# Kernel optimization log

Hardware: AMD Instinct MI355X
Metric: run time of the kernel (lower is better)

## Reference

```python
import jax, jax.numpy as jnp
import numpy as np

N_NODES = 150000
M_HYPEREDGES = 50000
N_TOTAL = N_NODES + M_HYPEREDGES
LATENT_DIM = 64
NUM_CLASS = 50
NNZ = 3_200_000
NUM_LAYERS = 3


def setup_inputs() -> dict:
    key = jax.random.key(0)
    k1, k2, k3, k4, k5, k6 = jax.random.split(key, 6)
    node_emb = 0.1 * jax.random.normal(k1, (N_NODES, LATENT_DIM), dtype=jnp.float32)
    hyper_emb = 0.1 * jax.random.normal(k2, (M_HYPEREDGES, LATENT_DIM), dtype=jnp.float32)
    W = jax.random.normal(k3, (LATENT_DIM, NUM_CLASS), dtype=jnp.float32) / np.sqrt(LATENT_DIM)
    b = jnp.zeros((NUM_CLASS,), dtype=jnp.float32)
    rows = jax.random.randint(k4, (NNZ,), 0, N_TOTAL, dtype=jnp.int32)
    cols = jax.random.randint(k5, (NNZ,), 0, N_TOTAL, dtype=jnp.int32)
    # normalized-adjacency-like small positive values
    vals = jax.random.uniform(k6, (NNZ,), dtype=jnp.float32) * 0.1
    return {"node_emb": node_emb, "hyper_emb": hyper_emb, "W": W, "b": b,
            "vals": vals, "rows": rows, "cols": cols}


def _spmm(vals, rows, cols, x):
    # y[r] = sum over edges (r, c): vals * x[c]   -- COO SpMM
    return jax.ops.segment_sum(vals[:, None] * x[cols], rows, num_segments=N_TOTAL)


def reference(node_emb, hyper_emb, W, b, vals, rows, cols):
    all_emb = jnp.concatenate([node_emb, hyper_emb], axis=0)  # [N, D]
    acc = all_emb  # running sum across layer embeddings (fused mean-pool)
    for _ in range(NUM_LAYERS):
        all_emb = _spmm(vals, rows, cols, all_emb)
        acc = acc + all_emb
    out = acc / (NUM_LAYERS + 1)          # mean over stacked layer embeddings
    nodes = out[:N_NODES]                 # split(out, [n_nodes, m_hyperedges])[0]
    Z = nodes @ W + b                     # linear head; dropout is identity in eval
    return jax.nn.log_softmax(Z, axis=1)
```

## Files before the change

kernel.cpp:

```cpp
#include <hip/hip_runtime.h>
#include <hip/hip_bf16.h>

#define N_NODES 150000
#define M_HYPER 50000
#define N_TOTAL 200000
#define DIM 64
#define NCLASS 50
#define NNZ 3200000

#define BSHIFT 9
#define BROWS 512
#define NBUK ((N_TOTAL + BROWS - 1) / BROWS)
#define EB 8192
#define CAP 9216

#define SCALE_UP 64.0f
#define SCALE_DN 0.015625f
#define VQ_ENC 163840.0f
#define VQ_DEC 6.103515625e-6f

typedef float v2f __attribute__((ext_vector_type(2)));

__global__ __launch_bounds__(512) void init_cur(int* __restrict__ bcur) {
    int t = threadIdx.x;
    if (t < NBUK) bcur[t] = t * CAP;
}

__global__ __launch_bounds__(1024) void bin_edges(
    const int* __restrict__ rows, const int* __restrict__ cols,
    const float* __restrict__ vals, int* __restrict__ bcur,
    int2* __restrict__ recs) {
    __shared__ int h[NBUK];
    __shared__ int lbase[NBUK];
    int base = blockIdx.x * EB;
    int cntE = NNZ - base; if (cntE > EB) cntE = EB;
    for (int i = threadIdx.x; i < NBUK; i += 1024) h[i] = 0;
    __syncthreads();
    for (int i = threadIdx.x; i < cntE; i += 1024)
        atomicAdd(&h[rows[base + i] >> BSHIFT], 1);
    __syncthreads();
    for (int i = threadIdx.x; i < NBUK; i += 1024) {
        int c = h[i];
        lbase[i] = c ? atomicAdd(&bcur[i], c) : 0;
    }
    __syncthreads();
    for (int i = threadIdx.x; i < NBUK; i += 1024) h[i] = 0;
    __syncthreads();
    for (int i = threadIdx.x; i < cntE; i += 1024) {
        int e = base + i;
        int r = rows[e];
        int b = r >> BSHIFT;
        int p = lbase[b] + atomicAdd(&h[b], 1);
        int q = __float2int_rn(vals[e] * VQ_ENC);
        if (q > 16383) q = 16383;
        if (p < NBUK * CAP)
            recs[p] = make_int2(((r & (BROWS - 1)) << 18) | cols[e], q);
    }
}

__global__ __launch_bounds__(512) void cnt_scan(const int* __restrict__ bcur,
                                                int* __restrict__ boff) {
    __shared__ int sh[512];
    int t = threadIdx.x;
    int c = (t < NBUK) ? (bcur[t] - t * CAP) : 0;
    sh[t] = c;
    __syncthreads();
    for (int off = 1; off < 512; off <<= 1) {
        int v = (t >= off) ? sh[t - off] : 0;
        __syncthreads();
        sh[t] += v;
        __syncthreads();
    }
    if (t < NBUK) boff[t] = sh[t] - c;
    if (t == 0) boff[NBUK] = NNZ;
}

__global__ __launch_bounds__(512) void build_csr(const int* __restrict__ boff,
                                                 const int2* __restrict__ recs,
                                                 int* __restrict__ row_ptr,
                                                 unsigned* __restrict__ edges) {
    __shared__ int h[BROWS * 8];
    __shared__ int ps[512];
    int b = blockIdx.x, t = threadIdx.x;
    int rbase = b * CAP;
    int obase = boff[b];
    int cnt = boff[b + 1] - obase;
    int row0 = b << BSHIFT;
    int nrows = N_TOTAL - row0;
    if (nrows > BROWS) nrows = BROWS;
    for (int i = t; i < BROWS * 8; i += 512) h[i] = 0;
    __syncthreads();
    for (int i = t; i < cnt; i += 512) {
        int rx = recs[rbase + i].x;
        int key = ((rx >> 18) << 3) | ((rx & 0x3FFFF) >> 15);
        atomicAdd(&h[key], 1);
    }
    __syncthreads();
    int loc[8];
    int s = 0;
#pragma unroll
    for (int j = 0; j < 8; ++j) { loc[j] = h[8 * t + j]; s += loc[j]; }
    ps[t] = s;
    __syncthreads();
    for (int off = 1; off < 512; off <<= 1) {
        int a = (t >= off) ? ps[t - off] : 0;
        __syncthreads();
        ps[t] += a;
        __syncthreads();
    }
    int run = obase + ((t == 0) ? 0 : ps[t - 1]);
    if (t < nrows) row_ptr[row0 + t] = run;
    if (b == NBUK - 1 && t == 0) row_ptr[N_TOTAL] = NNZ;
#pragma unroll
    for (int j = 0; j < 8; ++j) { h[8 * t + j] = run; run += loc[j]; }
    __syncthreads();
    for (int i = t; i < cnt; i += 512) {
        int2 rc = recs[rbase + i];
        int key = ((rc.x >> 18) << 3) | ((rc.x & 0x3FFFF) >> 15);
        int p = atomicAdd(&h[key], 1);
        edges[p] = (unsigned)(rc.x & 0x3FFFF) | ((unsigned)rc.y << 18);
    }
}

__global__ __launch_bounds__(256) void build_x_fp8(
    const float* __restrict__ node_emb, const float* __restrict__ hyper_emb,
    unsigned* __restrict__ xb) {
    int i = blockIdx.x * 256 + threadIdx.x;
    size_t base = (size_t)i * 4;
    const size_t NN = (size_t)N_NODES * DIM;
    if (base >= (size_t)N_TOTAL * DIM) return;
    float4 f;
    if (base < NN)
        f = *reinterpret_cast<const float4*>(node_emb + base);
    else
        f = *reinterpret_cast<const float4*>(hyper_emb + (base - NN));
    int lo = __builtin_amdgcn_cvt_pk_fp8_f32(f.x * SCALE_UP, f.y * SCALE_UP,
                                             0, false);
    int w = __builtin_amdgcn_cvt_pk_fp8_f32(f.z * SCALE_UP, f.w * SCALE_UP,
                                            lo, true);
    xb[i] = (unsigned)w;
}

__global__ __launch_bounds__(256) void spmm_gather(
    const int* __restrict__ row_ptr, const unsigned* __restrict__ edges,
    const unsigned char* __restrict__ x, unsigned char* __restrict__ y,
    int nrows) {
    int gid = blockIdx.x * 256 + threadIdx.x;
    int row = gid >> 4;
    int lane = threadIdx.x & 15;
    if (row >= nrows) return;
    int beg = row_ptr[row], end = row_ptr[row + 1];
    float a0 = 0.f, a1 = 0.f, a2 = 0.f, a3 = 0.f;
    int k = beg;
    for (; k + 7 < end; k += 8) {
        unsigned e[8];
        unsigned g[8];
#pragma unroll
        for (int j = 0; j < 8; ++j) e[j] = edges[k + j];
#pragma unroll
        for (int j = 0; j < 8; ++j)
            g[j] = *(const unsigned*)(x + ((size_t)(e[j] & 0x3FFFFu) << 6) + lane * 4);
#pragma unroll
        for (int j = 0; j < 8; ++j) {
            float v = (float)(e[j] >> 18) * VQ_DEC;
            v2f lo = __builtin_amdgcn_cvt_pk_f32_fp8((int)g[j], false);
            v2f hi = __builtin_amdgcn_cvt_pk_f32_fp8((int)g[j], true);
            a0 = fmaf(v, lo[0], a0);
            a1 = fmaf(v, lo[1], a1);
            a2 = fmaf(v, hi[0], a2);
            a3 = fmaf(v, hi[1], a3);
        }
    }
    for (; k + 3 < end; k += 4) {
        unsigned e[4];
        unsigned g[4];
#pragma unroll
        for (int j = 0; j < 4; ++j) e[j] = edges[k + j];
#pragma unroll
        for (int j = 0; j < 4; ++j)
            g[j] = *(const unsigned*)(x + ((size_t)(e[j] & 0x3FFFFu) << 6) + lane * 4);
#pragma unroll
        for (int j = 0; j < 4; ++j) {
            float v = (float)(e[j] >> 18) * VQ_DEC;
            v2f lo = __builtin_amdgcn_cvt_pk_f32_fp8((int)g[j], false);
            v2f hi = __builtin_amdgcn_cvt_pk_f32_fp8((int)g[j], true);
            a0 = fmaf(v, lo[0], a0);
            a1 = fmaf(v, lo[1], a1);
            a2 = fmaf(v, hi[0], a2);
            a3 = fmaf(v, hi[1], a3);
        }
    }
    for (; k < end; ++k) {
        unsigned e = edges[k];
        unsigned g = *(const unsigned*)(x + ((size_t)(e & 0x3FFFFu) << 6) + lane * 4);
        float v = (float)(e >> 18) * VQ_DEC;
        v2f lo = __builtin_amdgcn_cvt_pk_f32_fp8((int)g, false);
        v2f hi = __builtin_amdgcn_cvt_pk_f32_fp8((int)g, true);
        a0 = fmaf(v, lo[0], a0);
        a1 = fmaf(v, lo[1], a1);
        a2 = fmaf(v, hi[0], a2);
        a3 = fmaf(v, hi[1], a3);
    }
    int plo = __builtin_amdgcn_cvt_pk_fp8_f32(a0, a1, 0, false);
    int pk = __builtin_amdgcn_cvt_pk_fp8_f32(a2, a3, plo, true);
    *(unsigned*)(y + ((size_t)row << 6) + lane * 4) = (unsigned)pk;
}

__global__ __launch_bounds__(256) void classify(
    const float* __restrict__ node_emb, const unsigned char* __restrict__ y1,
    const unsigned char* __restrict__ y2,
    const unsigned char* __restrict__ y3, const float* __restrict__ W,
    const float* __restrict__ bias, float* __restrict__ Z) {
    int row = blockIdx.x * 256 + threadIdx.x;
    if (row >= N_NODES) return;
    const float4* np =
        reinterpret_cast<const float4*>(node_emb + (size_t)row * DIM);
    const unsigned* p1 = (const unsigned*)(y1 + ((size_t)row << 6));
    const unsigned* p2 = (const unsigned*)(y2 + ((size_t)row << 6));
    const unsigned* p3 = (const unsigned*)(y3 + ((size_t)row << 6));
    float xr[DIM];
#pragma unroll
    for (int i = 0; i < DIM / 4; ++i) {
        float4 f = np[i];
        unsigned w1 = p1[i], w2 = p2[i], w3 = p3[i];
        v2f a0 = __builtin_amdgcn_cvt_pk_f32_fp8((int)w1, false);
        v2f a1 = __builtin_amdgcn_cvt_pk_f32_fp8((int)w1, true);
        v2f b0 = __builtin_amdgcn_cvt_pk_f32_fp8((int)w2, false);
        v2f b1 = __builtin_amdgcn_cvt_pk_f32_fp8((int)w2, true);
        v2f c0 = __builtin_amdgcn_cvt_pk_f32_fp8((int)w3, false);
        v2f c1 = __builtin_amdgcn_cvt_pk_f32_fp8((int)w3, true);
        xr[4 * i + 0] = (f.x + (a0[0] + b0[0] + c0[0]) * SCALE_DN) * 0.25f;
        xr[4 * i + 1] = (f.y + (a0[1] + b0[1] + c0[1]) * SCALE_DN) * 0.25f;
        xr[4 * i + 2] = (f.z + (a1[0] + b1[0] + c1[0]) * SCALE_DN) * 0.25f;
        xr[4 * i + 3] = (f.w + (a1[1] + b1[1] + c1[1]) * SCALE_DN) * 0.25f;
    }
    float m = -1e30f, s = 0.f;
#pragma unroll 1
    for (int c = 0; c < NCLASS; ++c) {
        float d = bias[c];
#pragma unroll
        for (int k = 0; k < DIM; ++k) d = fmaf(xr[k], W[k * NCLASS + c], d);
        float mn = fmaxf(m, d);
        s = s * __expf(m - mn) + __expf(d - mn);
        m = mn;
    }
    float ls = m + __logf(s);
    float* zp = Z + (size_t)row * NCLASS;
#pragma unroll 1
    for (int c = 0; c < NCLASS; ++c) {
        float d = bias[c];
#pragma unroll
        for (int k = 0; k < DIM; ++k) d = fmaf(xr[k], W[k * NCLASS + c], d);
        zp[c] = d - ls;
    }
}

extern "C" void kernel_launch(void* const* d_in, const int* in_sizes, int n_in,
                              void* d_out, int out_size, void* d_ws, size_t ws_size,
                              hipStream_t stream) {
    const float* node_emb = (const float*)d_in[0];
    const float* hyper_emb = (const float*)d_in[1];
    const float* W = (const float*)d_in[2];
    const float* b = (const float*)d_in[3];
    const float* vals = (const float*)d_in[4];
    const int* rows = (const int*)d_in[5];
    const int* cols = (const int*)d_in[6];
    float* Z = (float*)d_out;

    const size_t BUF8 = (size_t)N_TOTAL * DIM;
    const size_t EDG = (size_t)NNZ * 4;

    char* w = (char*)d_ws;
    unsigned char* xb = (unsigned char*)w;  w += BUF8;
    unsigned char* y1 = (unsigned char*)w;  w += BUF8;
    unsigned char* y2 = (unsigned char*)w;  w += BUF8;
    unsigned char* y3 = (unsigned char*)w;  w += BUF8;
    unsigned* edges = (unsigned*)w;         w += EDG;
    int* row_ptr = (int*)w;                 w += (size_t)(N_TOTAL + 1) * 4;
    int* boff = (int*)w;                    w += 2048;
    int* bcur = (int*)w;                    w += 2048;
    int2* recs = (int2*)w;

    init_cur<<<1, 512, 0, stream>>>(bcur);
    const int bin_blocks = (NNZ + EB - 1) / EB;
    bin_edges<<<bin_blocks, 1024, 0, stream>>>(rows, cols, vals, bcur, recs);
    cnt_scan<<<1, 512, 0, stream>>>(bcur, boff);
    build_csr<<<NBUK, 512, 0, stream>>>(boff, recs, row_ptr, edges);

    const int cvt_blocks = (int)(((size_t)N_TOTAL * DIM / 4 + 255) / 256);
    build_x_fp8<<<cvt_blocks, 256, 0, stream>>>(node_emb, hyper_emb,
                                                (unsigned*)xb);

    const int out_blocks = (N_NODES + 255) / 256;
    const int full_blocks = (N_TOTAL * 16 + 255) / 256;
    const int node_blocks = (N_NODES * 16 + 255) / 256;

    spmm_gather<<<full_blocks, 256, 0, stream>>>(row_ptr, edges, xb, y1,
                                                 N_TOTAL);
    spmm_gather<<<full_blocks, 256, 0, stream>>>(row_ptr, edges, y1, y2,
                                                 N_TOTAL);
    spmm_gather<<<node_blocks, 256, 0, stream>>>(row_ptr, edges, y2, y3,
                                                 N_NODES);
    classify<<<out_blocks, 256, 0, stream>>>(node_emb, y1, y2, y3, W, b, Z);
}
```

Baseline: 293.2 us.

## Stage binned edges in LDS for coalesced writes; buffer classifier logits in shared memory

The binning kernel now sorts each block's edges by bucket in shared memory before writing them, so the writes to the global record array go out as contiguous runs instead of scattered stores. The record packing is reorganized so the full row index and the quantized value sit in one word and the column in the other, and the CSR build is updated to match. The classifier computes the logits once, keeps them in shared memory, and computes softmax over them, instead of evaluating the matrix product twice. It then writes the output tile coalesced. This adds about 64KB of LDS for staging in the binning kernel and about 51KB in the classifier, which may lower occupancy.

Result: faster. 263.0 us (-10.3%).

```diff
diff --git a/kernel.cpp b/kernel.cpp
--- a/kernel.cpp
+++ b/kernel.cpp
@@ -30,31 +30,51 @@
     const int* __restrict__ rows, const int* __restrict__ cols,
     const float* __restrict__ vals, int* __restrict__ bcur,
     int2* __restrict__ recs) {
+    __shared__ int2 stage[EB];
     __shared__ int h[NBUK];
-    __shared__ int lbase[NBUK];
+    __shared__ int lsb[NBUK];
+    __shared__ int lb[NBUK];
+    __shared__ int ps[512];
+    int t = threadIdx.x;
     int base = blockIdx.x * EB;
     int cntE = NNZ - base; if (cntE > EB) cntE = EB;
-    for (int i = threadIdx.x; i < NBUK; i += 1024) h[i] = 0;
-    __syncthreads();
-    for (int i = threadIdx.x; i < cntE; i += 1024)
+    for (int i = t; i < NBUK; i += 1024) h[i] = 0;
+    __syncthreads();
+    for (int i = t; i < cntE; i += 1024)
         atomicAdd(&h[rows[base + i] >> BSHIFT], 1);
     __syncthreads();
-    for (int i = threadIdx.x; i < NBUK; i += 1024) {
-        int c = h[i];
-        lbase[i] = c ? atomicAdd(&bcur[i], c) : 0;
-    }
-    __syncthreads();
-    for (int i = threadIdx.x; i < NBUK; i += 1024) h[i] = 0;
-    __syncthreads();
-    for (int i = threadIdx.x; i < cntE; i += 1024) {
+    if (t < 512) ps[t] = (t < NBUK) ? h[t] : 0;
+    __syncthreads();
+    for (int off = 1; off < 512; off <<= 1) {
+        int v = 0;
+        if (t < 512 && t >= off) v = ps[t - off];
+        __syncthreads();
+        if (t < 512) ps[t] += v;
+        __syncthreads();
+    }
+    if (t < NBUK) {
+        int c = h[t];
+        lsb[t] = ps[t] - c;
+        lb[t] = c ? atomicAdd(&bcur[t], c) : 0;
+    }
+    __syncthreads();
+    for (int i = t; i < NBUK; i += 1024) h[i] = 0;
+    __syncthreads();
+    for (int i = t; i < cntE; i += 1024) {
         int e = base + i;
         int r = rows[e];
         int b = r >> BSHIFT;
-        int p = lbase[b] + atomicAdd(&h[b], 1);
         int q = __float2int_rn(vals[e] * VQ_ENC);
         if (q > 16383) q = 16383;
-        if (p < NBUK * CAP)
-            recs[p] = make_int2(((r & (BROWS - 1)) << 18) | cols[e], q);
+        int p = lsb[b] + atomicAdd(&h[b], 1);
+        stage[p] = make_int2((int)(((unsigned)r << 14) | (unsigned)q), cols[e]);
+    }
+    __syncthreads();
+    for (int i = t; i < cntE; i += 1024) {
+        int2 rc = stage[i];
+        int b = (int)((unsigned)rc.x >> 14) >> BSHIFT;
+        int dst = lb[b] + (i - lsb[b]);
+        if (dst < NBUK * CAP) recs[dst] = rc;
     }
 }
 
@@ -91,8 +111,9 @@
     for (int i = t; i < BROWS * 8; i += 512) h[i] = 0;
     __syncthreads();
     for (int i = t; i < cnt; i += 512) {
-        int rx = recs[rbase + i].x;
-        int key = ((rx >> 18) << 3) | ((rx & 0x3FFFF) >> 15);
+        int2 rc = recs[rbase + i];
+        int rrel = (int)(((unsigned)rc.x >> 14) & (BROWS - 1));
+        int key = (rrel << 3) | (int)((unsigned)rc.y >> 15);
         atomicAdd(&h[key], 1);
     }
     __syncthreads();
@@ -116,9 +137,11 @@
     __syncthreads();
     for (int i = t; i < cnt; i += 512) {
         int2 rc = recs[rbase + i];
-        int key = ((rc.x >> 18) << 3) | ((rc.x & 0x3FFFF) >> 15);
+        unsigned rx = (unsigned)rc.x;
+        int rrel = (int)((rx >> 14) & (BROWS - 1));
+        int key = (rrel << 3) | (int)((unsigned)rc.y >> 15);
         int p = atomicAdd(&h[key], 1);
-        edges[p] = (unsigned)(rc.x & 0x3FFFF) | ((unsigned)rc.y << 18);
+        edges[p] = (unsigned)rc.y | ((rx & 0x3FFFu) << 18);
     }
 }
 
@@ -211,47 +234,58 @@
     const unsigned char* __restrict__ y2,
     const unsigned char* __restrict__ y3, const float* __restrict__ W,
     const float* __restrict__ bias, float* __restrict__ Z) {
-    int row = blockIdx.x * 256 + threadIdx.x;
-    if (row >= N_NODES) return;
-    const float4* np =
-        reinterpret_cast<const float4*>(node_emb + (size_t)row * DIM);
-    const unsigned* p1 = (const unsigned*)(y1 + ((size_t)row << 6));
-    const unsigned* p2 = (const unsigned*)(y2 + ((size_t)row << 6));
-    const unsigned* p3 = (const unsigned*)(y3 + ((size_t)row << 6));
-    float xr[DIM];
-#pragma unroll
-    for (int i = 0; i < DIM / 4; ++i) {
-        float4 f = np[i];
-        unsigned w1 = p1[i], w2 = p2[i], w3 = p3[i];
-        v2f a0 = __builtin_amdgcn_cvt_pk_f32_fp8((int)w1, false);
-        v2f a1 = __builtin_amdgcn_cvt_pk_f32_fp8((int)w1, true);
-        v2f b0 = __builtin_amdgcn_cvt_pk_f32_fp8((int)w2, false);
-        v2f b1 = __builtin_amdgcn_cvt_pk_f32_fp8((int)w2, true);
-        v2f c0 = __builtin_amdgcn_cvt_pk_f32_fp8((int)w3, false);
-        v2f c1 = __builtin_amdgcn_cvt_pk_f32_fp8((int)w3, true);
-        xr[4 * i + 0] = (f.x + (a0[0] + b0[0] + c0[0]) * SCALE_DN) * 0.25f;
-        xr[4 * i + 1] = (f.y + (a0[1] + b0[1] + c0[1]) * SCALE_DN) * 0.25f;
-        xr[4 * i + 2] = (f.z + (a1[0] + b1[0] + c1[0]) * SCALE_DN) * 0.25f;
-        xr[4 * i + 3] = (f.w + (a1[1] + b1[1] + c1[1]) * SCALE_DN) * 0.25f;
-    }
-    float m = -1e30f, s = 0.f;
+    __shared__ float zl[256 * 51];
+    int t = threadIdx.x;
+    int block_base = blockIdx.x * 256;
+    int row = block_base + t;
+    if (row < N_NODES) {
+        const float4* np =
+            reinterpret_cast<const float4*>(node_emb + (size_t)row * DIM);
+        const unsigned* p1 = (const unsigned*)(y1 + ((size_t)row << 6));
+        const unsigned* p2 = (const unsigned*)(y2 + ((size_t)row << 6));
+        const unsigned* p3 = (const unsigned*)(y3 + ((size_t)row << 6));
+        float xr[DIM];
+#pragma unroll
+        for (int i = 0; i < DIM / 4; ++i) {
+            float4 f = np[i];
+            unsigned w1 = p1[i], w2 = p2[i], w3 = p3[i];
+            v2f a0 = __builtin_amdgcn_cvt_pk_f32_fp8((int)w1, false);
+            v2f a1 = __builtin_amdgcn_cvt_pk_f32_fp8((int)w1, true);
+            v2f b0 = __builtin_amdgcn_cvt_pk_f32_fp8((int)w2, false);
+            v2f b1 = __builtin_amdgcn_cvt_pk_f32_fp8((int)w2, true);
+            v2f c0 = __builtin_amdgcn_cvt_pk_f32_fp8((int)w3, false);
+            v2f c1 = __builtin_amdgcn_cvt_pk_f32_fp8((int)w3, true);
+            xr[4 * i + 0] = (f.x + (a0[0] + b0[0] + c0[0]) * SCALE_DN) * 0.25f;
+            xr[4 * i + 1] = (f.y + (a0[1] + b0[1] + c0[1]) * SCALE_DN) * 0.25f;
+            xr[4 * i + 2] = (f.z + (a1[0] + b1[0] + c1[0]) * SCALE_DN) * 0.25f;
+            xr[4 * i + 3] = (f.w + (a1[1] + b1[1] + c1[1]) * SCALE_DN) * 0.25f;
+        }
+        float m = -1e30f;
 #pragma unroll 1
-    for (int c = 0; c < NCLASS; ++c) {
-        float d = bias[c];
-#pragma unroll
-        for (int k = 0; k < DIM; ++k) d = fmaf(xr[k], W[k * NCLASS + c], d);
-        float mn = fmaxf(m, d);
-        s = s * __expf(m - mn) + __expf(d - mn);
-        m = mn;
-    }
-    float ls = m + __logf(s);
-    float* zp = Z + (size_t)row * NCLASS;
+        for (int c = 0; c < NCLASS; ++c) {
+            float d = bias[c];
+#pragma unroll
+            for (int k = 0; k < DIM; ++k) d = fmaf(xr[k], W[k * NCLASS + c], d);
+            zl[t * 51 + c] = d;
+            m = fmaxf(m, d);
+        }
+        float s = 0.f;
 #pragma unroll 1
-    for (int c = 0; c < NCLASS; ++c) {
-        float d = bias[c];
-#pragma unroll
-        for (int k = 0; k < DIM; ++k) d = fmaf(xr[k], W[k * NCLASS + c], d);
-        zp[c] = d - ls;
+        for (int c = 0; c < NCLASS; ++c) s += __expf(zl[t * 51 + c] - m);
+        float ls = m + __logf(s);
+#pragma unroll 1
+        for (int c = 0; c < NCLASS; ++c) zl[t * 51 + c] -= ls;
+    }
+    __syncthreads();
+    int n_valid = N_NODES - block_base;
+    if (n_valid > 256) n_valid = 256;
+    if (n_valid < 0) n_valid = 0;
+    int total = n_valid * NCLASS;
+    float* zbase = Z + (size_t)block_base * NCLASS;
+    for (int i = t; i < total; i += 256) {
+        int r = i / NCLASS;
+        int c = i - r * NCLASS;
+        zbase[i] = zl[r * 51 + c];
     }
 }
 
```
